# Performance work log

Measured on AMD Instinct MI355X. Metric: run time of the kernel, lower is better.

The kernel has to match this reference:

```python
import jax, jax.numpy as jnp
import numpy as np

B, T, D_IN, D_OUT, R = 4, 4096, 2048, 2048, 64
SCALING = 2.0  # alpha / r = 128 / 64


def setup_inputs() -> dict:
    key = jax.random.key(0)
    k_x, k_w, k_a, k_b = jax.random.split(key, 4)
    x = jax.random.normal(k_x, (B, T, D_IN), dtype=jnp.float32)
    weight = jax.random.normal(k_w, (D_OUT, D_IN), dtype=jnp.float32) * 0.02
    lora_A = jax.random.normal(k_a, (R, D_IN), dtype=jnp.float32) * 0.02
    lora_B = jax.random.normal(k_b, (D_OUT, R), dtype=jnp.float32) * 0.02
    return {"x": x, "weight": weight, "lora_A": lora_A, "lora_B": lora_B}


def reference(x, weight, lora_A, lora_B):
    # Base (dequantized) linear: F.linear(x, W) with W [out, in]
    base = jnp.einsum("btd,od->bto", x, weight)
    # LoRA low-rank correction: scaling * (x @ A^T) @ B^T
    lora = jnp.einsum("btr,or->bto", jnp.einsum("btd,rd->btr", x, lora_A), lora_B)
    return base + SCALING * lora
```

## Files before the change

kernel.cpp:

```cpp
#include <hip/hip_runtime.h>
#include <hip/hip_bf16.h>


typedef short short8 __attribute__((ext_vector_type(8)));
typedef float f32x4 __attribute__((ext_vector_type(4)));

__device__ __forceinline__ unsigned short f2bf(float f) {
  unsigned u = __float_as_uint(f);
  u += 0x7fff + ((u >> 16) & 1);
  return (unsigned short)(u >> 16);
}

__global__ __launch_bounds__(256) void cvt_x_kernel(const float* __restrict__ x,
                                                    unsigned short* __restrict__ xb,
                                                    long long n) {
  long long idx = ((long long)blockIdx.x * 256 + threadIdx.x) * 8;
  long long stride = (long long)gridDim.x * 256 * 8;
  for (; idx < n; idx += stride) {
    float4 v0 = *(const float4*)(x + idx);
    float4 v1 = *(const float4*)(x + idx + 4);
    short8 o;
    o[0] = (short)f2bf(v0.x); o[1] = (short)f2bf(v0.y);
    o[2] = (short)f2bf(v0.z); o[3] = (short)f2bf(v0.w);
    o[4] = (short)f2bf(v1.x); o[5] = (short)f2bf(v1.y);
    o[6] = (short)f2bf(v1.z); o[7] = (short)f2bf(v1.w);
    *(short8*)(xb + idx) = o;
  }
}

__global__ __launch_bounds__(256) void weff_kernel(const float* __restrict__ W,
                                                   const float* __restrict__ Alora,
                                                   const float* __restrict__ Blora,
                                                   unsigned short* __restrict__ Weff,
                                                   int N, int K, int R, float scaling) {
  __shared__ float Bs[16][64];
  int t = threadIdx.x;
  int ob = blockIdx.y * 16;
  int i = blockIdx.x * 256 + t;
  for (int j = t; j < 16 * 64; j += 256)
    Bs[j >> 6][j & 63] = Blora[(ob + (j >> 6)) * R + (j & 63)];
  __syncthreads();
  float acc[16];
#pragma unroll
  for (int o = 0; o < 16; ++o) acc[o] = 0.f;
#pragma unroll 8
  for (int r = 0; r < 64; ++r) {
    float av = Alora[r * K + i];
#pragma unroll
    for (int o = 0; o < 16; ++o) acc[o] = fmaf(Bs[o][r], av, acc[o]);
  }
#pragma unroll
  for (int o = 0; o < 16; ++o) {
    float w = W[(size_t)(ob + o) * K + i];
    Weff[(size_t)(ob + o) * K + i] = f2bf(w + scaling * acc[o]);
  }
}

#define GLOAD_LDS16(g, l)                                                        \
  __builtin_amdgcn_global_load_lds((const __attribute__((address_space(1))) void*)(g), \
                                   (__attribute__((address_space(3))) void*)(l), 16, 0, 0)


__global__ __launch_bounds__(512, 2) void gemm8p_kernel(const unsigned short* __restrict__ Xb,
                                                        const unsigned short* __restrict__ Wb,
                                                        float* __restrict__ out,
                                                        int M, int N, int K) {
  __shared__ __align__(16) char lds[131072];

  const int t = threadIdx.x;
  const int lane = t & 63;
  const int w = t >> 6;
  const int wr = w >> 2, wc = w & 3;

  const int nwg = gridDim.x, cpx = nwg >> 3;
  const int swz = (blockIdx.x & 7) * cpx + (blockIdx.x >> 3);
  const int nbn = N >> 8;
  const int bm = swz / nbn, bn = swz % nbn;

  f32x4 acc[8][4];
  const f32x4 z = {0.f, 0.f, 0.f, 0.f};
#pragma unroll
  for (int i = 0; i < 8; ++i)
#pragma unroll
    for (int j = 0; j < 4; ++j) acc[i][j] = z;

  const int srow = (t >> 2) ^ ((t >> 5) & 1);
  const int scol = ((t & 3) ^ ((t >> 3) & 3)) * 8;
  const unsigned short* gA = Xb + (size_t)(bm * 256 + srow) * K + scol;
  const unsigned short* gB = Wb + (size_t)(bn * 256 + srow) * K + scol;

  const int lane15 = lane & 15, ksl = lane >> 4;
  const int key = ((lane15 >> 1) & 7) << 4;
  const int aRead = (((wr * 128 + lane15) * 64) + ksl * 16) ^ key;
  const int bRead = (((wc * 64 + lane15) * 64) + ksl * 16) ^ key;

  short8 af0, af1, af2, af3, bf0, bf1, bf2, bf3;

#define STG_A(NS, KSU, KOFF)                                                    \
  GLOAD_LDS16(gA + (KOFF), lds + (NS) * 65536 + (KSU) * 16384 + t * 16);        \
  GLOAD_LDS16(gA + (size_t)128 * K + (KOFF),                                    \
              lds + (NS) * 65536 + (KSU) * 16384 + 8192 + t * 16);
#define STG_B(NS, KSU, KOFF)                                                    \
  GLOAD_LDS16(gB + (KOFF), lds + (NS) * 65536 + 32768 + (KSU) * 16384 + t * 16);\
  GLOAD_LDS16(gB + (size_t)128 * K + (KOFF),                                    \
              lds + (NS) * 65536 + 32768 + (KSU) * 16384 + 8192 + t * 16);

#define RD_A(SLOT, KSU, MB) {                                                   \
    const char* p_ = lds + (SLOT) * 65536 + (KSU) * 16384 + aRead + (MB) * 1024;\
    af0 = *(const short8*)(p_);                                                 \
    af1 = *(const short8*)(p_ + 1024);                                          \
    af2 = *(const short8*)(p_ + 2048);                                          \
    af3 = *(const short8*)(p_ + 3072); }
#define RD_B(SLOT, KSU) {                                                       \
    const char* p_ = lds + (SLOT) * 65536 + 32768 + (KSU) * 16384 + bRead;      \
    bf0 = *(const short8*)(p_);                                                 \
    bf1 = *(const short8*)(p_ + 1024);                                          \
    bf2 = *(const short8*)(p_ + 2048);                                          \
    bf3 = *(const short8*)(p_ + 3072); }

#define MM4(AF, MI)                                                             \
  acc[MI][0] = __builtin_amdgcn_mfma_f32_16x16x32_bf16(AF, bf0, acc[MI][0], 0, 0, 0); \
  acc[MI][1] = __builtin_amdgcn_mfma_f32_16x16x32_bf16(AF, bf1, acc[MI][1], 0, 0, 0); \
  acc[MI][2] = __builtin_amdgcn_mfma_f32_16x16x32_bf16(AF, bf2, acc[MI][2], 0, 0, 0); \
  acc[MI][3] = __builtin_amdgcn_mfma_f32_16x16x32_bf16(AF, bf3, acc[MI][3], 0, 0, 0);

#define PH(SLOT, KSU, MB, RDB_STMT, STG_STMT, WAIT_STMT)                        \
  RD_A(SLOT, KSU, MB)                                                           \
  RDB_STMT                                                                      \
  STG_STMT                                                                      \
  WAIT_STMT                                                                     \
  __builtin_amdgcn_s_barrier();                                                 \
  asm volatile("s_waitcnt lgkmcnt(0)" ::: "memory");                            \
  __builtin_amdgcn_sched_barrier(0);                                            \
  __builtin_amdgcn_s_setprio(1);                                                \
  MM4(af0, (MB) + 0) MM4(af1, (MB) + 1) MM4(af2, (MB) + 2) MM4(af3, (MB) + 3)   \
  __builtin_amdgcn_s_setprio(0);                                                \
  __builtin_amdgcn_s_barrier();

#define VM4 asm volatile("s_waitcnt vmcnt(4)" ::: "memory");
#define VM0 asm volatile("s_waitcnt vmcnt(0)" ::: "memory");
#define NOP_

#define KTILE(SLOT, NS, KNEXT)                                                  \
  PH(SLOT, 0, 0, RD_B(SLOT, 0), STG_A(NS, 0, KNEXT), NOP_)                      \
  PH(SLOT, 0, 4, NOP_,          STG_B(NS, 0, KNEXT), VM4)                       \
  PH(SLOT, 1, 0, RD_B(SLOT, 1), STG_A(NS, 1, (KNEXT) + 32), NOP_)               \
  PH(SLOT, 1, 4, NOP_,          STG_B(NS, 1, (KNEXT) + 32), VM4)

#define KTILE_LAST(SLOT)                                                        \
  PH(SLOT, 0, 0, RD_B(SLOT, 0), NOP_, NOP_)                                     \
  PH(SLOT, 0, 4, NOP_,          NOP_, VM0)                                      \
  PH(SLOT, 1, 0, RD_B(SLOT, 1), NOP_, NOP_)                                     \
  PH(SLOT, 1, 4, NOP_,          NOP_, NOP_)

  STG_A(0, 0, 0) STG_B(0, 0, 0) STG_A(0, 1, 32) STG_B(0, 1, 32)
  VM4
  __builtin_amdgcn_s_barrier();

  int kk = 64;
#pragma unroll 1
  for (int it = 0; it < 15; ++it) {
    KTILE(0, 1, kk) kk += 64;
    KTILE(1, 0, kk) kk += 64;
  }
  KTILE(0, 1, kk)
  KTILE_LAST(1)

  const int orow0 = bm * 256 + wr * 128 + ksl * 4;
  const int ocol0 = bn * 256 + wc * 64 + lane15;
#pragma unroll
  for (int i = 0; i < 8; ++i)
#pragma unroll
    for (int j = 0; j < 4; ++j) {
      size_t base = (size_t)(orow0 + i * 16) * N + (ocol0 + j * 16);
#pragma unroll
      for (int q = 0; q < 4; ++q) out[base + (size_t)q * N] = acc[i][j][q];
    }
}

extern "C" void kernel_launch(void* const* d_in, const int* in_sizes, int n_in,
                              void* d_out, int out_size, void* d_ws, size_t ws_size,
                              hipStream_t stream) {
  const float* x  = (const float*)d_in[0];
  const float* W  = (const float*)d_in[1];
  const float* Al = (const float*)d_in[2];
  const float* Bl = (const float*)d_in[3];
  float* out = (float*)d_out;

  const int K = 2048;
  const long long M = (long long)in_sizes[0] / K;
  const int N = in_sizes[1] / K;
  const int R = in_sizes[2] / K;

  unsigned short* xb   = (unsigned short*)d_ws;
  unsigned short* weff = xb + (size_t)M * K;

  cvt_x_kernel<<<2048, 256, 0, stream>>>(x, xb, (long long)M * K);
  weff_kernel<<<dim3(K / 256, N / 16), 256, 0, stream>>>(W, Al, Bl, weff, N, K, R, 2.0f);
  gemm8p_kernel<<<(N / 256) * (int)(M / 256), 512, 0, stream>>>(xb, weff, out, (int)M, N, K);
}
```

Before: 389.1 us.

## Switch GEMM inner loop from 16x16x32 to 32x32x16 bf16 MFMA tiles

Replaces the 16x16x32 MFMA micro-tiling with 32x32x16 MFMA instructions. Each wave now computes a 128x64 block as 4x2 32x32 tiles, which cuts LDS fragment reads per MFMA and issues fewer, larger matrix instructions. Each k-tile is split into four phases that each read A and B fragments, and the trailing barrier after each compute phase is removed. The output store and LDS swizzle addressing are rewritten for the 32x32 accumulator layout, and the dropped barrier carries a risk of LDS read/write races between phases.

```diff
diff --git a/kernel.cpp b/kernel.cpp
--- a/kernel.cpp
+++ b/kernel.cpp
@@ -3,7 +3,7 @@
 
 
 typedef short short8 __attribute__((ext_vector_type(8)));
-typedef float f32x4 __attribute__((ext_vector_type(4)));
+typedef float f32x16 __attribute__((ext_vector_type(16)));
 
 __device__ __forceinline__ unsigned short f2bf(float f) {
   unsigned u = __float_as_uint(f);
@@ -61,7 +61,7 @@
                                    (__attribute__((address_space(3))) void*)(l), 16, 0, 0)
 
 
-__global__ __launch_bounds__(512, 2) void gemm8p_kernel(const unsigned short* __restrict__ Xb,
+__global__ __launch_bounds__(512, 2) void gemm32_kernel(const unsigned short* __restrict__ Xb,
                                                         const unsigned short* __restrict__ Wb,
                                                         float* __restrict__ out,
                                                         int M, int N, int K) {
@@ -77,24 +77,27 @@
   const int nbn = N >> 8;
   const int bm = swz / nbn, bn = swz % nbn;
 
-  f32x4 acc[8][4];
-  const f32x4 z = {0.f, 0.f, 0.f, 0.f};
-#pragma unroll
-  for (int i = 0; i < 8; ++i)
-#pragma unroll
-    for (int j = 0; j < 4; ++j) acc[i][j] = z;
+  f32x16 acc[4][2];
+#pragma unroll
+  for (int i = 0; i < 4; ++i)
+#pragma unroll
+    for (int j = 0; j < 2; ++j)
+#pragma unroll
+      for (int q = 0; q < 16; ++q) acc[i][j][q] = 0.f;
 
   const int srow = (t >> 2) ^ ((t >> 5) & 1);
   const int scol = ((t & 3) ^ ((t >> 3) & 3)) * 8;
   const unsigned short* gA = Xb + (size_t)(bm * 256 + srow) * K + scol;
   const unsigned short* gB = Wb + (size_t)(bn * 256 + srow) * K + scol;
 
-  const int lane15 = lane & 15, ksl = lane >> 4;
-  const int key = ((lane15 >> 1) & 7) << 4;
-  const int aRead = (((wr * 128 + lane15) * 64) + ksl * 16) ^ key;
-  const int bRead = (((wc * 64 + lane15) * 64) + ksl * 16) ^ key;
-
-  short8 af0, af1, af2, af3, bf0, bf1, bf2, bf3;
+  const int lane31 = lane & 31, lhalf = lane >> 5;
+  const int key = ((lane31 >> 1) & 7) << 4;
+  const int linA = ((wr * 128 + lane31) * 64) + lhalf * 16;
+  const int linB = ((wc * 64 + lane31) * 64) + lhalf * 16;
+  const int aswz0 = linA ^ key,        aswz1 = (linA + 32) ^ key;
+  const int bswz0 = linB ^ key,        bswz1 = (linB + 32) ^ key;
+
+  short8 af0, af1, af2, af3, bf0, bf1;
 
 #define STG_A(NS, KSU, KOFF)                                                    \
   GLOAD_LDS16(gA + (KOFF), lds + (NS) * 65536 + (KSU) * 16384 + t * 16);        \
@@ -105,53 +108,54 @@
   GLOAD_LDS16(gB + (size_t)128 * K + (KOFF),                                    \
               lds + (NS) * 65536 + 32768 + (KSU) * 16384 + 8192 + t * 16);
 
-#define RD_A(SLOT, KSU, MB) {                                                   \
-    const char* p_ = lds + (SLOT) * 65536 + (KSU) * 16384 + aRead + (MB) * 1024;\
-    af0 = *(const short8*)(p_);                                                 \
-    af1 = *(const short8*)(p_ + 1024);                                          \
-    af2 = *(const short8*)(p_ + 2048);                                          \
-    af3 = *(const short8*)(p_ + 3072); }
-#define RD_B(SLOT, KSU) {                                                       \
-    const char* p_ = lds + (SLOT) * 65536 + 32768 + (KSU) * 16384 + bRead;      \
-    bf0 = *(const short8*)(p_);                                                 \
-    bf1 = *(const short8*)(p_ + 1024);                                          \
-    bf2 = *(const short8*)(p_ + 2048);                                          \
-    bf3 = *(const short8*)(p_ + 3072); }
-
-#define MM4(AF, MI)                                                             \
-  acc[MI][0] = __builtin_amdgcn_mfma_f32_16x16x32_bf16(AF, bf0, acc[MI][0], 0, 0, 0); \
-  acc[MI][1] = __builtin_amdgcn_mfma_f32_16x16x32_bf16(AF, bf1, acc[MI][1], 0, 0, 0); \
-  acc[MI][2] = __builtin_amdgcn_mfma_f32_16x16x32_bf16(AF, bf2, acc[MI][2], 0, 0, 0); \
-  acc[MI][3] = __builtin_amdgcn_mfma_f32_16x16x32_bf16(AF, bf3, acc[MI][3], 0, 0, 0);
-
-#define PH(SLOT, KSU, MB, RDB_STMT, STG_STMT, WAIT_STMT)                        \
-  RD_A(SLOT, KSU, MB)                                                           \
-  RDB_STMT                                                                      \
+#define RD32(SLOT, KQ) {                                                        \
+    const char* pa_ = lds + (SLOT) * 65536 + ((KQ) >> 1) * 16384                \
+                      + (((KQ) & 1) ? aswz1 : aswz0);                           \
+    af0 = *(const short8*)(pa_);                                                \
+    af1 = *(const short8*)(pa_ + 2048);                                         \
+    af2 = *(const short8*)(pa_ + 4096);                                         \
+    af3 = *(const short8*)(pa_ + 6144);                                         \
+    const char* pb_ = lds + (SLOT) * 65536 + 32768 + ((KQ) >> 1) * 16384        \
+                      + (((KQ) & 1) ? bswz1 : bswz0);                           \
+    bf0 = *(const short8*)(pb_);                                                \
+    bf1 = *(const short8*)(pb_ + 2048); }
+
+#define MM8                                                                     \
+  acc[0][0] = __builtin_amdgcn_mfma_f32_32x32x16_bf16(af0, bf0, acc[0][0], 0, 0, 0); \
+  acc[0][1] = __builtin_amdgcn_mfma_f32_32x32x16_bf16(af0, bf1, acc[0][1], 0, 0, 0); \
+  acc[1][0] = __builtin_amdgcn_mfma_f32_32x32x16_bf16(af1, bf0, acc[1][0], 0, 0, 0); \
+  acc[1][1] = __builtin_amdgcn_mfma_f32_32x32x16_bf16(af1, bf1, acc[1][1], 0, 0, 0); \
+  acc[2][0] = __builtin_amdgcn_mfma_f32_32x32x16_bf16(af2, bf0, acc[2][0], 0, 0, 0); \
+  acc[2][1] = __builtin_amdgcn_mfma_f32_32x32x16_bf16(af2, bf1, acc[2][1], 0, 0, 0); \
+  acc[3][0] = __builtin_amdgcn_mfma_f32_32x32x16_bf16(af3, bf0, acc[3][0], 0, 0, 0); \
+  acc[3][1] = __builtin_amdgcn_mfma_f32_32x32x16_bf16(af3, bf1, acc[3][1], 0, 0, 0);
+
+#define VM4 asm volatile("s_waitcnt vmcnt(4)" ::: "memory");
+#define VM0 asm volatile("s_waitcnt vmcnt(0)" ::: "memory");
+#define NOP_
+
+#define PH32(SLOT, KQ, STG_STMT, WAIT_STMT)                                     \
+  RD32(SLOT, KQ)                                                                \
   STG_STMT                                                                      \
   WAIT_STMT                                                                     \
   __builtin_amdgcn_s_barrier();                                                 \
   asm volatile("s_waitcnt lgkmcnt(0)" ::: "memory");                            \
   __builtin_amdgcn_sched_barrier(0);                                            \
   __builtin_amdgcn_s_setprio(1);                                                \
-  MM4(af0, (MB) + 0) MM4(af1, (MB) + 1) MM4(af2, (MB) + 2) MM4(af3, (MB) + 3)   \
-  __builtin_amdgcn_s_setprio(0);                                                \
-  __builtin_amdgcn_s_barrier();
-
-#define VM4 asm volatile("s_waitcnt vmcnt(4)" ::: "memory");
-#define VM0 asm volatile("s_waitcnt vmcnt(0)" ::: "memory");
-#define NOP_
-
-#define KTILE(SLOT, NS, KNEXT)                                                  \
-  PH(SLOT, 0, 0, RD_B(SLOT, 0), STG_A(NS, 0, KNEXT), NOP_)                      \
-  PH(SLOT, 0, 4, NOP_,          STG_B(NS, 0, KNEXT), VM4)                       \
-  PH(SLOT, 1, 0, RD_B(SLOT, 1), STG_A(NS, 1, (KNEXT) + 32), NOP_)               \
-  PH(SLOT, 1, 4, NOP_,          STG_B(NS, 1, (KNEXT) + 32), VM4)
-
-#define KTILE_LAST(SLOT)                                                        \
-  PH(SLOT, 0, 0, RD_B(SLOT, 0), NOP_, NOP_)                                     \
-  PH(SLOT, 0, 4, NOP_,          NOP_, VM0)                                      \
-  PH(SLOT, 1, 0, RD_B(SLOT, 1), NOP_, NOP_)                                     \
-  PH(SLOT, 1, 4, NOP_,          NOP_, NOP_)
+  MM8                                                                           \
+  __builtin_amdgcn_s_setprio(0);
+
+#define KTILE32(SLOT, NS, KNEXT)                                                \
+  PH32(SLOT, 0, STG_A(NS, 0, KNEXT), NOP_)                                      \
+  PH32(SLOT, 1, STG_B(NS, 0, KNEXT), VM4)                                       \
+  PH32(SLOT, 2, STG_A(NS, 1, (KNEXT) + 32), NOP_)                               \
+  PH32(SLOT, 3, STG_B(NS, 1, (KNEXT) + 32), VM4)
+
+#define KTILE32_LAST(SLOT)                                                      \
+  PH32(SLOT, 0, NOP_, NOP_)                                                     \
+  PH32(SLOT, 1, NOP_, VM0)                                                      \
+  PH32(SLOT, 2, NOP_, NOP_)                                                     \
+  PH32(SLOT, 3, NOP_, NOP_)
 
   STG_A(0, 0, 0) STG_B(0, 0, 0) STG_A(0, 1, 32) STG_B(0, 1, 32)
   VM4
@@ -160,21 +164,24 @@
   int kk = 64;
 #pragma unroll 1
   for (int it = 0; it < 15; ++it) {
-    KTILE(0, 1, kk) kk += 64;
-    KTILE(1, 0, kk) kk += 64;
-  }
-  KTILE(0, 1, kk)
-  KTILE_LAST(1)
-
-  const int orow0 = bm * 256 + wr * 128 + ksl * 4;
-  const int ocol0 = bn * 256 + wc * 64 + lane15;
-#pragma unroll
-  for (int i = 0; i < 8; ++i)
-#pragma unroll
-    for (int j = 0; j < 4; ++j) {
-      size_t base = (size_t)(orow0 + i * 16) * N + (ocol0 + j * 16);
-#pragma unroll
-      for (int q = 0; q < 4; ++q) out[base + (size_t)q * N] = acc[i][j][q];
+    KTILE32(0, 1, kk) kk += 64;
+    KTILE32(1, 0, kk) kk += 64;
+  }
+  KTILE32(0, 1, kk)
+  KTILE32_LAST(1)
+
+  const int orow0 = bm * 256 + wr * 128 + lhalf * 4;
+  const int ocol0 = bn * 256 + wc * 64 + lane31;
+#pragma unroll
+  for (int i = 0; i < 4; ++i)
+#pragma unroll
+    for (int j = 0; j < 2; ++j) {
+#pragma unroll
+      for (int reg = 0; reg < 16; ++reg) {
+        int row = orow0 + i * 32 + (reg & 3) + 8 * (reg >> 2);
+        int col = ocol0 + j * 32;
+        out[(size_t)row * N + col] = acc[i][j][reg];
+      }
     }
 }
 
@@ -197,5 +204,5 @@
 
   cvt_x_kernel<<<2048, 256, 0, stream>>>(x, xb, (long long)M * K);
   weff_kernel<<<dim3(K / 256, N / 16), 256, 0, stream>>>(W, Al, Bl, weff, N, K, R, 2.0f);
-  gemm8p_kernel<<<(N / 256) * (int)(M / 256), 512, 0, stream>>>(xb, weff, out, (int)M, N, K);
-}
+  gemm32_kernel<<<(N / 256) * (int)(M / 256), 512, 0, stream>>>(xb, weff, out, (int)M, N, K);
+}
```

After: 396.7 us. No clear change (+2.0%).
